# Optimization experiments

Hardware: AMD Instinct MI355X
Metric: run time of the kernel (lower is better)

The kernel has to match this reference:

```python
import jax, jax.numpy as jnp
import numpy as np

N_NODES = 170000
N_EDGES = 1200000
IN_DIM = 64
OUT_DIM = 40


def setup_inputs() -> dict:
    key = jax.random.key(0)
    k1, k2, k3, k4 = jax.random.split(key, 4)
    feats = jax.random.normal(k1, (N_NODES, IN_DIM), dtype=jnp.float32)
    # Linear layer params (Kaiming-ish scale)
    W = jax.random.normal(k2, (OUT_DIM, IN_DIM), dtype=jnp.float32) * (1.0 / np.sqrt(IN_DIM))
    b = jnp.zeros((OUT_DIM,), dtype=jnp.float32)
    src = jax.random.randint(k3, (N_EDGES,), 0, N_NODES, dtype=jnp.int64)
    dst = jax.random.randint(k4, (N_EDGES,), 0, N_NODES, dtype=jnp.int64)
    return {"feats": feats, "W": W, "b": b, "src": src, "dst": dst}


def reference(feats, W, b, src, dst):
    # DGL SGConv, k=1: symmetric normalization by in-degree^-1/2 on both sides.
    n = feats.shape[0]
    deg = jax.ops.segment_sum(jnp.ones_like(dst, dtype=feats.dtype), dst, num_segments=n)
    norm = jax.lax.rsqrt(jnp.maximum(deg, 1.0))  # clamp(min=1)
    h = feats * norm[:, None]                    # [N, D] pre-scale
    msgs = jnp.take(h, src, axis=0)              # [E, D] gather
    agg = jax.ops.segment_sum(msgs, dst, num_segments=n)  # [N, D] scatter-sum
    h = agg * norm[:, None]                      # post-scale
    out = jnp.einsum('nd,cd->nc', h, W) + b      # Linear(IN_DIM -> OUT_DIM)
    return out
```

## Files before the change

kernel.cpp:

```cpp
#include <hip/hip_runtime.h>
#include <hip/hip_bf16.h>

#define N_NODES 170000
#define N_EDGES 1200000
#define IN_DIM 64
#define OUT_DIM 40
#define PAD 32
#define ZW 20
#define MTILES (N_NODES / 16)
#define SEGS 8
#define SEG_SZ (N_NODES / SEGS)
#define SLICES 512
#define SLICE_E ((N_EDGES + SLICES - 1) / SLICES)

typedef __attribute__((ext_vector_type(8))) short short8;
typedef __attribute__((ext_vector_type(4))) float f32x4;

__device__ __forceinline__ float bf2f(unsigned int u) {
    union { unsigned int i; float f; } v;
    v.i = u << 16;
    return v.f;
}

__device__ __forceinline__ unsigned short f2bf_bits(float x) {
    __hip_bfloat16 h = __float2bfloat16(x);
    union { __hip_bfloat16 h; unsigned short u; } c; c.h = h;
    return c.u;
}

__device__ __forceinline__ int load_idx(const void* p, int e, int is_i32) {
    return is_i32 ? ((const int*)p)[e] : (int)((const long long*)p)[e];
}

__global__ void k_sniff_convert(const unsigned short* __restrict__ Wraw,
                                const unsigned short* __restrict__ braw,
                                const unsigned int* __restrict__ dstraw,
                                int* __restrict__ flags,
                                float* __restrict__ Wf, float* __restrict__ bf) {
    __shared__ int s_f32, s_i32;
    if (threadIdx.x == 0) { s_f32 = 0; s_i32 = 0; }
    __syncthreads();
    for (int i = threadIdx.x; i < OUT_DIM * IN_DIM; i += blockDim.x) {
        float v = bf2f(Wraw[i]);
        if (!(fabsf(v) <= 100.0f)) atomicOr(&s_f32, 1);
    }
    for (int i = threadIdx.x; i < 256; i += blockDim.x) {
        if (dstraw[2 * i + 1] != 0u) atomicOr(&s_i32, 1);
    }
    __syncthreads();
    int is_f32 = s_f32;
    if (threadIdx.x == 0) { flags[0] = s_f32; flags[1] = s_i32; }
    for (int i = threadIdx.x; i < OUT_DIM * IN_DIM; i += blockDim.x)
        Wf[i] = is_f32 ? ((const float*)Wraw)[i] : bf2f(Wraw[i]);
    for (int i = threadIdx.x; i < OUT_DIM; i += blockDim.x)
        bf[i] = is_f32 ? ((const float*)braw)[i] : bf2f(braw[i]);
}

__global__ void __launch_bounds__(256) k_fill(
    const void* __restrict__ src, const void* __restrict__ dst,
    int* __restrict__ cnt, int* __restrict__ slots,
    const int* __restrict__ flags) {
    int is_i32 = flags[1];
    int seg   = blockIdx.x & 7;
    int slice = blockIdx.x >> 3;
    int lo = seg * SEG_SZ, hi = lo + SEG_SZ;
    int e0 = slice * SLICE_E;
    int e1 = e0 + SLICE_E; if (e1 > N_EDGES) e1 = N_EDGES;
    for (int e = e0 + (int)threadIdx.x; e < e1; e += 256) {
        int d = load_idx(dst, e, is_i32);
        if (d >= lo && d < hi) {
            int s = load_idx(src, e, is_i32);
            int pos = atomicAdd(&cnt[d], 1);
            if (pos < PAD) slots[(size_t)d * PAD + pos] = s;
        }
    }
}

__global__ void __launch_bounds__(256) k_transform_mfma(
    const void* __restrict__ feats, const float* __restrict__ Wf,
    const int* __restrict__ cnt, unsigned short* __restrict__ Zp16,
    const int* __restrict__ flags) {
    int is_f32 = flags[0];
    int wave = (blockIdx.x * blockDim.x + threadIdx.x) >> 6;
    int lane = threadIdx.x & 63;
    if (wave >= MTILES) return;
    int m = lane & 15;
    int quad = lane >> 4;
    int node0 = wave * 16;

    short8 a0, a1;
    if (is_f32) {
        const float* frow = (const float*)feats + (size_t)(node0 + m) * IN_DIM + quad * 8;
        float4 p0 = *(const float4*)(frow + 0);
        float4 p1 = *(const float4*)(frow + 4);
        float4 p2 = *(const float4*)(frow + 32);
        float4 p3 = *(const float4*)(frow + 36);
        a0[0] = (short)f2bf_bits(p0.x); a0[1] = (short)f2bf_bits(p0.y);
        a0[2] = (short)f2bf_bits(p0.z); a0[3] = (short)f2bf_bits(p0.w);
        a0[4] = (short)f2bf_bits(p1.x); a0[5] = (short)f2bf_bits(p1.y);
        a0[6] = (short)f2bf_bits(p1.z); a0[7] = (short)f2bf_bits(p1.w);
        a1[0] = (short)f2bf_bits(p2.x); a1[1] = (short)f2bf_bits(p2.y);
        a1[2] = (short)f2bf_bits(p2.z); a1[3] = (short)f2bf_bits(p2.w);
        a1[4] = (short)f2bf_bits(p3.x); a1[5] = (short)f2bf_bits(p3.y);
        a1[6] = (short)f2bf_bits(p3.z); a1[7] = (short)f2bf_bits(p3.w);
    } else {
        const unsigned short* frow = (const unsigned short*)feats + (size_t)(node0 + m) * IN_DIM + quad * 8;
        ushort4 q0 = *(const ushort4*)(frow + 0);
        ushort4 q1 = *(const ushort4*)(frow + 4);
        ushort4 q2 = *(const ushort4*)(frow + 32);
        ushort4 q3 = *(const ushort4*)(frow + 36);
        a0[0] = (short)q0.x; a0[1] = (short)q0.y; a0[2] = (short)q0.z; a0[3] = (short)q0.w;
        a0[4] = (short)q1.x; a0[5] = (short)q1.y; a0[6] = (short)q1.z; a0[7] = (short)q1.w;
        a1[0] = (short)q2.x; a1[1] = (short)q2.y; a1[2] = (short)q2.z; a1[3] = (short)q2.w;
        a1[4] = (short)q3.x; a1[5] = (short)q3.y; a1[6] = (short)q3.z; a1[7] = (short)q3.w;
    }

    f32x4 c0 = {0.f, 0.f, 0.f, 0.f}, c1 = c0, c2 = c0;
#pragma unroll
    for (int t = 0; t < 3; t++) {
        int n = t * 16 + m;
        bool ok = (n < OUT_DIM);
        const float* wrow = Wf + (size_t)(ok ? n : 0) * IN_DIM + quad * 8;
        short8 b0, b1;
#pragma unroll
        for (int j = 0; j < 8; j++) { b0[j] = 0; b1[j] = 0; }
        if (ok) {
            float4 w0 = *(const float4*)(wrow + 0);
            float4 w1 = *(const float4*)(wrow + 4);
            float4 w2 = *(const float4*)(wrow + 32);
            float4 w3 = *(const float4*)(wrow + 36);
            b0[0] = (short)f2bf_bits(w0.x); b0[1] = (short)f2bf_bits(w0.y);
            b0[2] = (short)f2bf_bits(w0.z); b0[3] = (short)f2bf_bits(w0.w);
            b0[4] = (short)f2bf_bits(w1.x); b0[5] = (short)f2bf_bits(w1.y);
            b0[6] = (short)f2bf_bits(w1.z); b0[7] = (short)f2bf_bits(w1.w);
            b1[0] = (short)f2bf_bits(w2.x); b1[1] = (short)f2bf_bits(w2.y);
            b1[2] = (short)f2bf_bits(w2.z); b1[3] = (short)f2bf_bits(w2.w);
            b1[4] = (short)f2bf_bits(w3.x); b1[5] = (short)f2bf_bits(w3.y);
            b1[6] = (short)f2bf_bits(w3.z); b1[7] = (short)f2bf_bits(w3.w);
        }
        if (t == 0) {
            c0 = __builtin_amdgcn_mfma_f32_16x16x32_bf16(a0, b0, c0, 0, 0, 0);
            c0 = __builtin_amdgcn_mfma_f32_16x16x32_bf16(a1, b1, c0, 0, 0, 0);
        } else if (t == 1) {
            c1 = __builtin_amdgcn_mfma_f32_16x16x32_bf16(a0, b0, c1, 0, 0, 0);
            c1 = __builtin_amdgcn_mfma_f32_16x16x32_bf16(a1, b1, c1, 0, 0, 0);
        } else {
            c2 = __builtin_amdgcn_mfma_f32_16x16x32_bf16(a0, b0, c2, 0, 0, 0);
            c2 = __builtin_amdgcn_mfma_f32_16x16x32_bf16(a1, b1, c2, 0, 0, 0);
        }
    }

    int r0 = quad * 4;
    float nv[4];
#pragma unroll
    for (int r = 0; r < 4; r++) {
        int dg = cnt[node0 + r0 + r];
        nv[r] = rsqrtf(dg > 1 ? (float)dg : 1.0f);
    }
#pragma unroll
    for (int r = 0; r < 4; r++) {
        size_t base = (size_t)(node0 + r0 + r) * OUT_DIM;
        Zp16[base + m]      = f2bf_bits(c0[r] * nv[r]);
        Zp16[base + 16 + m] = f2bf_bits(c1[r] * nv[r]);
        if (m < 8)
            Zp16[base + 32 + m] = f2bf_bits(c2[r] * nv[r]);
    }
}

__global__ void __launch_bounds__(256) k_gather(
    const int* __restrict__ cnt, const int* __restrict__ slots,
    const unsigned int* __restrict__ Zp, const float* __restrict__ bf,
    float* __restrict__ out) {
    int wid = (blockIdx.x * blockDim.x + threadIdx.x) >> 6;
    int lane = threadIdx.x & 63;
    if (wid >= N_NODES) return;
    int deg = cnt[wid];
    int dc = deg > PAD ? PAD : deg;
    const int* sl = slots + (size_t)wid * PAD;
    int myslot = sl[lane & 31];

    int grp = lane / 10;
    int cidx = lane - grp * 10;
    bool lact = (grp < 6);

    float a0 = 0.f, a1 = 0.f, a2 = 0.f, a3 = 0.f;
    if (dc > 0) {
        int rounds = (dc + 5) / 6;
        bool v = lact && (grp < dc);
        int s = __shfl(myslot, (v ? grp : 0) & 31);
        uint2 r = *(const uint2*)(Zp + (size_t)s * ZW + 2 * cidx);
        for (int rd = 1; rd < rounds; rd++) {
            int e1 = rd * 6 + grp;
            bool v1 = lact && (e1 < dc);
            int s1 = __shfl(myslot, (v1 ? e1 : 0) & 31);
            uint2 rn = *(const uint2*)(Zp + (size_t)s1 * ZW + 2 * cidx);
            if (v) {
                a0 += bf2f(r.x & 0xFFFFu); a1 += bf2f(r.x >> 16);
                a2 += bf2f(r.y & 0xFFFFu); a3 += bf2f(r.y >> 16);
            }
            v = v1; r = rn;
        }
        if (v) {
            a0 += bf2f(r.x & 0xFFFFu); a1 += bf2f(r.x >> 16);
            a2 += bf2f(r.y & 0xFFFFu); a3 += bf2f(r.y >> 16);
        }
    }
    float b0 = a0 + __shfl(a0, (lane + 30) & 63);
    float b1 = a1 + __shfl(a1, (lane + 30) & 63);
    float b2 = a2 + __shfl(a2, (lane + 30) & 63);
    float b3 = a3 + __shfl(a3, (lane + 30) & 63);
    float t0 = b0 + __shfl(b0, (lane + 10) & 63) + __shfl(b0, (lane + 20) & 63);
    float t1 = b1 + __shfl(b1, (lane + 10) & 63) + __shfl(b1, (lane + 20) & 63);
    float t2 = b2 + __shfl(b2, (lane + 10) & 63) + __shfl(b2, (lane + 20) & 63);
    float t3 = b3 + __shfl(b3, (lane + 10) & 63) + __shfl(b3, (lane + 20) & 63);
    if (lane < 10) {
        float nv = rsqrtf(deg > 1 ? (float)deg : 1.0f);
        float4 o;
        o.x = fmaf(t0, nv, bf[4 * lane + 0]);
        o.y = fmaf(t1, nv, bf[4 * lane + 1]);
        o.z = fmaf(t2, nv, bf[4 * lane + 2]);
        o.w = fmaf(t3, nv, bf[4 * lane + 3]);
        *reinterpret_cast<float4*>(out + (size_t)wid * OUT_DIM + 4 * lane) = o;
    }
}

extern "C" void kernel_launch(void* const* d_in, const int* in_sizes, int n_in,
                              void* d_out, int out_size, void* d_ws, size_t ws_size,
                              hipStream_t stream) {
    const void* feats = d_in[0];
    const void* W     = d_in[1];
    const void* b     = d_in[2];
    const void* src   = d_in[3];
    const void* dst   = d_in[4];

    char* ws = (char*)d_ws;
    int*            flags = (int*)(ws + 0);
    float*          bf    = (float*)(ws + 256);
    float*          Wf    = (float*)(ws + 1024);
    int*            cnt   = (int*)(ws + 16384);
    int*            slots = (int*)(ws + 696448);
    unsigned short* Zp16  = (unsigned short*)(ws + 22456448);
    unsigned int*   Zp    = (unsigned int*)(ws + 22456448);

    (void)hipMemsetAsync(cnt, 0, 680000, stream);

    k_sniff_convert<<<1, 256, 0, stream>>>((const unsigned short*)W, (const unsigned short*)b,
                                           (const unsigned int*)dst, flags, Wf, bf);
    k_fill<<<SLICES * SEGS, 256, 0, stream>>>(src, dst, cnt, slots, flags);
    k_transform_mfma<<<(MTILES * 64 + 255) / 256, 256, 0, stream>>>(feats, Wf, cnt, Zp16, flags);
    k_gather<<<(N_NODES * 64 + 255) / 256, 256, 0, stream>>>(cnt, slots, Zp, bf, (float*)d_out);
}
```

Before: 223.3 us.

## Replace segmented edge scan with two-pass XCC-local bucketing and work-stealing fill

Result: slower. 786.1 us (+252.0%).

```diff
diff --git a/kernel.cpp b/kernel.cpp
--- a/kernel.cpp
+++ b/kernel.cpp
@@ -10,8 +10,10 @@
 #define MTILES (N_NODES / 16)
 #define SEGS 8
 #define SEG_SZ (N_NODES / SEGS)
-#define SLICES 512
-#define SLICE_E ((N_EDGES + SLICES - 1) / SLICES)
+#define BCAP 32768
+#define CH 1024
+#define NBLK_A 1024
+#define NBLK_B 512
 
 typedef __attribute__((ext_vector_type(8))) short short8;
 typedef __attribute__((ext_vector_type(4))) float f32x4;
@@ -28,59 +30,103 @@
     return c.u;
 }
 
-__device__ __forceinline__ int load_idx(const void* p, int e, int is_i32) {
-    return is_i32 ? ((const int*)p)[e] : (int)((const long long*)p)[e];
-}
-
-__global__ void k_sniff_convert(const unsigned short* __restrict__ Wraw,
-                                const unsigned short* __restrict__ braw,
-                                const unsigned int* __restrict__ dstraw,
-                                int* __restrict__ flags,
-                                float* __restrict__ Wf, float* __restrict__ bf) {
-    __shared__ int s_f32, s_i32;
-    if (threadIdx.x == 0) { s_f32 = 0; s_i32 = 0; }
-    __syncthreads();
-    for (int i = threadIdx.x; i < OUT_DIM * IN_DIM; i += blockDim.x) {
-        float v = bf2f(Wraw[i]);
-        if (!(fabsf(v) <= 100.0f)) atomicOr(&s_f32, 1);
-    }
-    for (int i = threadIdx.x; i < 256; i += blockDim.x) {
-        if (dstraw[2 * i + 1] != 0u) atomicOr(&s_i32, 1);
-    }
-    __syncthreads();
-    int is_f32 = s_f32;
-    if (threadIdx.x == 0) { flags[0] = s_f32; flags[1] = s_i32; }
-    for (int i = threadIdx.x; i < OUT_DIM * IN_DIM; i += blockDim.x)
-        Wf[i] = is_f32 ? ((const float*)Wraw)[i] : bf2f(Wraw[i]);
-    for (int i = threadIdx.x; i < OUT_DIM; i += blockDim.x)
-        bf[i] = is_f32 ? ((const float*)braw)[i] : bf2f(braw[i]);
-}
-
-__global__ void __launch_bounds__(256) k_fill(
+__global__ void __launch_bounds__(256) k_bucket(
     const void* __restrict__ src, const void* __restrict__ dst,
     int* __restrict__ cnt, int* __restrict__ slots,
-    const int* __restrict__ flags) {
-    int is_i32 = flags[1];
-    int seg   = blockIdx.x & 7;
-    int slice = blockIdx.x >> 3;
-    int lo = seg * SEG_SZ, hi = lo + SEG_SZ;
-    int e0 = slice * SLICE_E;
-    int e1 = e0 + SLICE_E; if (e1 > N_EDGES) e1 = N_EDGES;
-    for (int e = e0 + (int)threadIdx.x; e < e1; e += 256) {
-        int d = load_idx(dst, e, is_i32);
-        if (d >= lo && d < hi) {
-            int s = load_idx(src, e, is_i32);
-            int pos = atomicAdd(&cnt[d], 1);
-            if (pos < PAD) slots[(size_t)d * PAD + pos] = s;
+    uint2* __restrict__ bucket, int* __restrict__ cursor) {
+    int lane = threadIdx.x & 63;
+
+    unsigned int oddw = ((const unsigned int*)dst)[2 * lane + 1];
+    bool is_i32 = (__ballot(oddw != 0u) != 0ull);
+
+    unsigned int xcc;
+    asm volatile("s_getreg_b32 %0, hwreg(HW_REG_XCC_ID, 0, 32)" : "=s"(xcc));
+    xcc &= 7;
+
+    const int stride = NBLK_A * 256;
+    int e0 = blockIdx.x * 256 + threadIdx.x;
+    const int iters = (N_EDGES + stride - 1) / stride;
+
+    for (int it = 0; it < iters; it++) {
+        int e = e0 + it * stride;
+        bool valid = (e < N_EDGES);
+        int d = 0, s = 0;
+        if (valid) {
+            if (is_i32) {
+                d = ((const int*)dst)[e];
+                s = ((const int*)src)[e];
+            } else {
+                d = (int)((const long long*)dst)[e];
+                s = (int)((const long long*)src)[e];
+            }
+        }
+        int sg = valid ? (int)((float)d * (8.0f / 170000.0f)) : -1;
+        if (sg > 7) sg = 7;
+#pragma unroll
+        for (int g = 0; g < 8; g++) {
+            unsigned long long m = __ballot(sg == g);
+            if (m == 0ull) continue;
+            int leader = __ffsll((unsigned long long)m) - 1;
+            int cg = __popcll(m);
+            int base = 0;
+            if (lane == leader) base = atomicAdd(&cursor[(xcc << 3) + g], cg);
+            base = __shfl(base, leader);
+            if (sg == g) {
+                int rank = __popcll(m & ((1ull << lane) - 1ull));
+                int pos = base + rank;
+                if (pos < BCAP) {
+                    bucket[(size_t)((xcc << 3) + g) * BCAP + pos] = make_uint2((unsigned)d, (unsigned)s);
+                } else {
+                    int p2 = atomicAdd(&cnt[d], 1);
+                    if (p2 < PAD) slots[(size_t)d * PAD + p2] = s;
+                }
+            }
+        }
+    }
+}
+
+__global__ void __launch_bounds__(256) k_fillB(
+    int* __restrict__ cnt, int* __restrict__ slots,
+    const uint2* __restrict__ bucket, const int* __restrict__ cursor,
+    int* __restrict__ tick) {
+    unsigned int xcc;
+    asm volatile("s_getreg_b32 %0, hwreg(HW_REG_XCC_ID, 0, 32)" : "=s"(xcc));
+    xcc &= 7;
+    __shared__ int s_t;
+    for (int sweep = 0; sweep < SEGS; sweep++) {
+        int seg = (xcc + sweep) & 7;
+        int pre[8]; int tot = 0;
+#pragma unroll
+        for (int x = 0; x < 8; x++) {
+            int l = cursor[(x << 3) + seg];
+            if (l > BCAP) l = BCAP;
+            pre[x] = tot; tot += l;
+        }
+        int nchunks = (tot + CH - 1) / CH;
+        for (;;) {
+            if (threadIdx.x == 0) s_t = atomicAdd(&tick[seg], 1);
+            __syncthreads();
+            int t = s_t;
+            __syncthreads();
+            if (t >= nchunks) break;
+            int base = t * CH;
+            int end = base + CH; if (end > tot) end = tot;
+            for (int i = base + (int)threadIdx.x; i < end; i += 256) {
+                int x = 0;
+#pragma unroll
+                for (int j = 1; j < 8; j++) if (i >= pre[j]) x = j;
+                uint2 ds = bucket[(size_t)((x << 3) + seg) * BCAP + (i - pre[x])];
+                int d = (int)ds.x;
+                int p = atomicAdd(&cnt[d], 1);
+                if (p < PAD) slots[(size_t)d * PAD + p] = (int)ds.y;
+            }
         }
     }
 }
 
 __global__ void __launch_bounds__(256) k_transform_mfma(
-    const void* __restrict__ feats, const float* __restrict__ Wf,
-    const int* __restrict__ cnt, unsigned short* __restrict__ Zp16,
-    const int* __restrict__ flags) {
-    int is_f32 = flags[0];
+    const float* __restrict__ feats, const float* __restrict__ W,
+    const int* __restrict__ cnt, unsigned short* __restrict__ Zp16) {
     int wave = (blockIdx.x * blockDim.x + threadIdx.x) >> 6;
     int lane = threadIdx.x & 63;
     if (wave >= MTILES) return;
@@ -88,39 +134,27 @@
     int quad = lane >> 4;
     int node0 = wave * 16;
 
+    const float* frow = feats + (size_t)(node0 + m) * IN_DIM + quad * 8;
+    float4 p0 = *(const float4*)(frow + 0);
+    float4 p1 = *(const float4*)(frow + 4);
+    float4 p2 = *(const float4*)(frow + 32);
+    float4 p3 = *(const float4*)(frow + 36);
     short8 a0, a1;
-    if (is_f32) {
-        const float* frow = (const float*)feats + (size_t)(node0 + m) * IN_DIM + quad * 8;
-        float4 p0 = *(const float4*)(frow + 0);
-        float4 p1 = *(const float4*)(frow + 4);
-        float4 p2 = *(const float4*)(frow + 32);
-        float4 p3 = *(const float4*)(frow + 36);
-        a0[0] = (short)f2bf_bits(p0.x); a0[1] = (short)f2bf_bits(p0.y);
-        a0[2] = (short)f2bf_bits(p0.z); a0[3] = (short)f2bf_bits(p0.w);
-        a0[4] = (short)f2bf_bits(p1.x); a0[5] = (short)f2bf_bits(p1.y);
-        a0[6] = (short)f2bf_bits(p1.z); a0[7] = (short)f2bf_bits(p1.w);
-        a1[0] = (short)f2bf_bits(p2.x); a1[1] = (short)f2bf_bits(p2.y);
-        a1[2] = (short)f2bf_bits(p2.z); a1[3] = (short)f2bf_bits(p2.w);
-        a1[4] = (short)f2bf_bits(p3.x); a1[5] = (short)f2bf_bits(p3.y);
-        a1[6] = (short)f2bf_bits(p3.z); a1[7] = (short)f2bf_bits(p3.w);
-    } else {
-        const unsigned short* frow = (const unsigned short*)feats + (size_t)(node0 + m) * IN_DIM + quad * 8;
-        ushort4 q0 = *(const ushort4*)(frow + 0);
-        ushort4 q1 = *(const ushort4*)(frow + 4);
-        ushort4 q2 = *(const ushort4*)(frow + 32);
-        ushort4 q3 = *(const ushort4*)(frow + 36);
-        a0[0] = (short)q0.x; a0[1] = (short)q0.y; a0[2] = (short)q0.z; a0[3] = (short)q0.w;
-        a0[4] = (short)q1.x; a0[5] = (short)q1.y; a0[6] = (short)q1.z; a0[7] = (short)q1.w;
-        a1[0] = (short)q2.x; a1[1] = (short)q2.y; a1[2] = (short)q2.z; a1[3] = (short)q2.w;
-        a1[4] = (short)q3.x; a1[5] = (short)q3.y; a1[6] = (short)q3.z; a1[7] = (short)q3.w;
-    }
+    a0[0] = (short)f2bf_bits(p0.x); a0[1] = (short)f2bf_bits(p0.y);
+    a0[2] = (short)f2bf_bits(p0.z); a0[3] = (short)f2bf_bits(p0.w);
+    a0[4] = (short)f2bf_bits(p1.x); a0[5] = (short)f2bf_bits(p1.y);
+    a0[6] = (short)f2bf_bits(p1.z); a0[7] = (short)f2bf_bits(p1.w);
+    a1[0] = (short)f2bf_bits(p2.x); a1[1] = (short)f2bf_bits(p2.y);
+    a1[2] = (short)f2bf_bits(p2.z); a1[3] = (short)f2bf_bits(p2.w);
+    a1[4] = (short)f2bf_bits(p3.x); a1[5] = (short)f2bf_bits(p3.y);
+    a1[6] = (short)f2bf_bits(p3.z); a1[7] = (short)f2bf_bits(p3.w);
 
     f32x4 c0 = {0.f, 0.f, 0.f, 0.f}, c1 = c0, c2 = c0;
 #pragma unroll
     for (int t = 0; t < 3; t++) {
         int n = t * 16 + m;
         bool ok = (n < OUT_DIM);
-        const float* wrow = Wf + (size_t)(ok ? n : 0) * IN_DIM + quad * 8;
+        const float* wrow = W + (size_t)(ok ? n : 0) * IN_DIM + quad * 8;
         short8 b0, b1;
 #pragma unroll
         for (int j = 0; j < 8; j++) { b0[j] = 0; b1[j] = 0; }
@@ -169,7 +203,7 @@
 
 __global__ void __launch_bounds__(256) k_gather(
     const int* __restrict__ cnt, const int* __restrict__ slots,
-    const unsigned int* __restrict__ Zp, const float* __restrict__ bf,
+    const unsigned int* __restrict__ Zp, const float* __restrict__ b,
     float* __restrict__ out) {
     int wid = (blockIdx.x * blockDim.x + threadIdx.x) >> 6;
     int lane = threadIdx.x & 63;
@@ -216,10 +250,10 @@
     if (lane < 10) {
         float nv = rsqrtf(deg > 1 ? (float)deg : 1.0f);
         float4 o;
-        o.x = fmaf(t0, nv, bf[4 * lane + 0]);
-        o.y = fmaf(t1, nv, bf[4 * lane + 1]);
-        o.z = fmaf(t2, nv, bf[4 * lane + 2]);
-        o.w = fmaf(t3, nv, bf[4 * lane + 3]);
+        o.x = fmaf(t0, nv, b[4 * lane + 0]);
+        o.y = fmaf(t1, nv, b[4 * lane + 1]);
+        o.z = fmaf(t2, nv, b[4 * lane + 2]);
+        o.w = fmaf(t3, nv, b[4 * lane + 3]);
         *reinterpret_cast<float4*>(out + (size_t)wid * OUT_DIM + 4 * lane) = o;
     }
 }
@@ -227,26 +261,25 @@
 extern "C" void kernel_launch(void* const* d_in, const int* in_sizes, int n_in,
                               void* d_out, int out_size, void* d_ws, size_t ws_size,
                               hipStream_t stream) {
-    const void* feats = d_in[0];
-    const void* W     = d_in[1];
-    const void* b     = d_in[2];
-    const void* src   = d_in[3];
-    const void* dst   = d_in[4];
+    const float* feats = (const float*)d_in[0];
+    const float* W     = (const float*)d_in[1];
+    const float* b     = (const float*)d_in[2];
+    const void*  src   = d_in[3];
+    const void*  dst   = d_in[4];
 
     char* ws = (char*)d_ws;
-    int*            flags = (int*)(ws + 0);
-    float*          bf    = (float*)(ws + 256);
-    float*          Wf    = (float*)(ws + 1024);
-    int*            cnt   = (int*)(ws + 16384);
-    int*            slots = (int*)(ws + 696448);
-    unsigned short* Zp16  = (unsigned short*)(ws + 22456448);
-    unsigned int*   Zp    = (unsigned int*)(ws + 22456448);
-
-    (void)hipMemsetAsync(cnt, 0, 680000, stream);
-
-    k_sniff_convert<<<1, 256, 0, stream>>>((const unsigned short*)W, (const unsigned short*)b,
-                                           (const unsigned int*)dst, flags, Wf, bf);
-    k_fill<<<SLICES * SEGS, 256, 0, stream>>>(src, dst, cnt, slots, flags);
-    k_transform_mfma<<<(MTILES * 64 + 255) / 256, 256, 0, stream>>>(feats, Wf, cnt, Zp16, flags);
-    k_gather<<<(N_NODES * 64 + 255) / 256, 256, 0, stream>>>(cnt, slots, Zp, bf, (float*)d_out);
-}
+    int*            cnt    = (int*)(ws + 16384);
+    int*            cursor = (int*)(ws + 696384);
+    int*            tick   = (int*)(ws + 696640);
+    int*            slots  = (int*)(ws + 696704);
+    unsigned short* Zp16   = (unsigned short*)(ws + 22456704);
+    unsigned int*   Zp     = (unsigned int*)(ws + 22456704);
+    uint2*          bucket = (uint2*)(ws + 36056704);
+
+    (void)hipMemsetAsync(ws + 16384, 0, 680000 + 256 + 32, stream);
+
+    k_bucket<<<NBLK_A, 256, 0, stream>>>(src, dst, cnt, slots, bucket, cursor);
+    k_fillB<<<NBLK_B, 256, 0, stream>>>(cnt, slots, bucket, cursor, tick);
+    k_transform_mfma<<<(MTILES * 64 + 255) / 256, 256, 0, stream>>>(feats, W, cnt, Zp16);
+    k_gather<<<(N_NODES * 64 + 255) / 256, 256, 0, stream>>>(cnt, slots, Zp, b, (float*)d_out);
+}
```
